# Kernel optimization log

Measured on AMD Instinct MI355X. Metric: run time of the kernel, lower is better.

The kernel has to match this reference:

```python
import jax, jax.numpy as jnp
import numpy as np

N = 320
C_Z = 128
H = 4
C_H = 32


def setup_inputs() -> dict:
    key = jax.random.key(0)
    ks = jax.random.split(key, 9)
    s = 0.02
    return {
        "x_normed": jax.random.normal(ks[0], (1, N, N, C_Z), dtype=jnp.float32),
        "triangle_bias": jax.random.normal(ks[1], (1, 1, H, N, N), dtype=jnp.float32),
        "wq": jax.random.normal(ks[2], (C_Z, H * C_H), dtype=jnp.float32) * s,
        "wk": jax.random.normal(ks[3], (C_Z, H * C_H), dtype=jnp.float32) * s,
        "wv": jax.random.normal(ks[4], (C_Z, H * C_H), dtype=jnp.float32) * s,
        "wg": jax.random.normal(ks[5], (C_Z, H * C_H), dtype=jnp.float32) * s,
        "bg": jnp.ones((H * C_H,), dtype=jnp.float32),  # OpenFold gating bias init = 1
        "wo": jax.random.normal(ks[6], (H * C_H, C_Z), dtype=jnp.float32) * s,
        "bo": jnp.zeros((C_Z,), dtype=jnp.float32),
    }


def reference(x_normed, triangle_bias, wq, wk, wv, wg, bg, wo, bo):
    b, n, m, cz = x_normed.shape  # [1, N, N, C_Z]
    # q/k/v projections (no bias, per OpenFold Attention)
    q = (x_normed @ wq).reshape(b, n, m, H, C_H) / np.sqrt(C_H)
    k = (x_normed @ wk).reshape(b, n, m, H, C_H)
    v = (x_normed @ wv).reshape(b, n, m, H, C_H)
    # attention over the last row dim; first N is a batch dim.
    # scores: [b, n, H, q, k]; triangle_bias [1, 1, H, N, N] broadcasts over n.
    scores = jnp.einsum("bnqhc,bnkhc->bnhqk", q, k) + triangle_bias
    a = jax.nn.softmax(scores, axis=-1)
    o = jnp.einsum("bnhqk,bnkhc->bnqhc", a, v)
    # sigmoid output gating
    g = jax.nn.sigmoid((x_normed @ wg + bg).reshape(b, n, m, H, C_H))
    o = o * g
    out = o.reshape(b, n, m, H * C_H) @ wo + bo
    return out
```

## Files before the change

kernel.cpp:

```cpp
#include <hip/hip_runtime.h>

typedef __bf16 bf16;
typedef __bf16 bf16x8 __attribute__((ext_vector_type(8)));
typedef __bf16 bf16x4 __attribute__((ext_vector_type(4)));
typedef __bf16 bf16x2 __attribute__((ext_vector_type(2)));
typedef float  f32x4  __attribute__((ext_vector_type(4)));
typedef unsigned int u32;
typedef u32 u32x4 __attribute__((ext_vector_type(4)));

#define NN_  320
#define CZ_  128
#define H_   4
#define CH_  32
#define LOG2E_ 1.4426950408889634f

__device__ __forceinline__ u32 pack_bf16(float a, float b) {
    bf16x2 t; t[0] = (bf16)a; t[1] = (bf16)b;
    return __builtin_bit_cast(u32, t);
}

__global__ __launch_bounds__(512) void qkvg_kernel(
    const float* __restrict__ x,
    const float* __restrict__ wq, const float* __restrict__ wk,
    const float* __restrict__ wv, const float* __restrict__ wg,
    const float* __restrict__ bg,
    bf16* __restrict__ Qp, bf16* __restrict__ Kp,
    bf16* __restrict__ Vp, bf16* __restrict__ Gp)
{
    __shared__ bf16 wl[128][136];
    const int tid  = threadIdx.x;
    const int lane = tid & 63, wid = tid >> 6;
    const int l15  = lane & 15, l4 = lane >> 4;
    const int m0   = blockIdx.x << 7;

    const int arow = m0 + wid * 16 + l15;
    bf16x8 xf[4];
    #pragma unroll
    for (int ks = 0; ks < 4; ++ks) {
        float4 f0 = *reinterpret_cast<const float4*>(x + (size_t)arow * CZ_ + ks * 32 + l4 * 8);
        float4 f1 = *reinterpret_cast<const float4*>(x + (size_t)arow * CZ_ + ks * 32 + l4 * 8 + 4);
        bf16x8 t;
        t[0]=(bf16)f0.x; t[1]=(bf16)f0.y; t[2]=(bf16)f0.z; t[3]=(bf16)f0.w;
        t[4]=(bf16)f1.x; t[5]=(bf16)f1.y; t[6]=(bf16)f1.z; t[7]=(bf16)f1.w;
        xf[ks] = t;
    }

    int nQ[4], qQ[4];
    #pragma unroll
    for (int r = 0; r < 4; ++r) {
        int m = m0 + wid * 16 + l4 * 4 + r;
        nQ[r] = m / NN_; qQ[r] = m - nQ[r] * NN_;
    }
    const int nV = arow / NN_, qV = arow - nV * NN_;

    const float* Ws[4] = {wq, wk, wv, wg};
    #pragma unroll
    for (int mat = 0; mat < 4; ++mat) {
        __syncthreads();
        const float* w = Ws[mat];
        #pragma unroll
        for (int it = 0; it < 8; ++it) {
            int u  = tid + (it << 9);
            int j  = u & 127, k4 = u >> 7;
            bf16x4 t;
            t[0] = (bf16)w[(k4 * 4 + 0) * CZ_ + j];
            t[1] = (bf16)w[(k4 * 4 + 1) * CZ_ + j];
            t[2] = (bf16)w[(k4 * 4 + 2) * CZ_ + j];
            t[3] = (bf16)w[(k4 * 4 + 3) * CZ_ + j];
            *reinterpret_cast<bf16x4*>(&wl[j][k4 * 4]) = t;
        }
        __syncthreads();

        f32x4 zero = {0.f, 0.f, 0.f, 0.f};
        f32x4 acc[8];
        #pragma unroll
        for (int ct = 0; ct < 8; ++ct) acc[ct] = zero;

        #pragma unroll
        for (int ks = 0; ks < 4; ++ks) {
            #pragma unroll
            for (int ct = 0; ct < 8; ++ct) {
                bf16x8 wf = *reinterpret_cast<const bf16x8*>(&wl[ct * 16 + l15][ks * 32 + l4 * 8]);
                if (mat == 2)
                    acc[ct] = __builtin_amdgcn_mfma_f32_16x16x32_bf16(wf, xf[ks], acc[ct], 0, 0, 0);
                else
                    acc[ct] = __builtin_amdgcn_mfma_f32_16x16x32_bf16(xf[ks], wf, acc[ct], 0, 0, 0);
            }
        }

        if (mat == 0) {
            #pragma unroll
            for (int ct = 0; ct < 8; ++ct) {
                const int cout = ct * 16 + l15, hh = cout >> 5, cc = cout & 31;
                #pragma unroll
                for (int r = 0; r < 4; ++r)
                    Qp[(size_t)((nQ[r] * H_ + hh) * NN_ + qQ[r]) * CH_ + cc] =
                        (bf16)(acc[ct][r] * 0.25500003540695464f);
            }
        } else if (mat == 1) {
            #pragma unroll
            for (int ct = 0; ct < 8; ++ct) {
                const int cout = ct * 16 + l15, hh = cout >> 5, cc = cout & 31;
                #pragma unroll
                for (int r = 0; r < 4; ++r)
                    Kp[(size_t)((nQ[r] * H_ + hh) * NN_ + qQ[r]) * CH_ + cc] = (bf16)acc[ct][r];
            }
        } else if (mat == 2) {
            #pragma unroll
            for (int ct = 0; ct < 8; ++ct) {
                #pragma unroll
                for (int r = 0; r < 4; ++r) {
                    const int cout = ct * 16 + l4 * 4 + r, hh = cout >> 5, cc = cout & 31;
                    Vp[(size_t)((nV * H_ + hh) * CH_ + cc) * NN_ + qV] = (bf16)acc[ct][r];
                }
            }
        } else {
            #pragma unroll
            for (int ct = 0; ct < 8; ++ct) {
                const int cout = ct * 16 + l15;
                const float bgj = bg[cout];
                #pragma unroll
                for (int r = 0; r < 4; ++r) {
                    float t = acc[ct][r] + bgj;
                    Gp[(size_t)(m0 + wid * 16 + l4 * 4 + r) * CZ_ + cout] =
                        (bf16)(1.0f / (1.0f + __expf(-t)));
                }
            }
        }
    }
}

__global__ __launch_bounds__(640, 2) void attn_kernel(
    const bf16* __restrict__ Qp, const bf16* __restrict__ Kp,
    const bf16* __restrict__ Vp, bf16* __restrict__ Gp,
    const float* __restrict__ bias)
{
    __shared__ bf16 Kl[320][40];
    __shared__ bf16 Vl[32][344];
    const int tid  = threadIdx.x;
    const int lane = tid & 63;
    const int wid  = tid >> 6;
    const int l15  = lane & 15, l4 = lane >> 4;
    const int gid = blockIdx.x;
    const int lin = (gid & 7) * 160 + (gid >> 3);
    const int h   = lin / NN_;
    const int n   = lin - h * NN_;

    const size_t nh = (size_t)(n * H_ + h);
    const bf16* Kh = Kp + nh * NN_ * CH_;
    const bf16* Vh = Vp + nh * CH_ * NN_;
    const bf16* Qh = Qp + nh * NN_ * CH_;

    #pragma unroll
    for (int i = 0; i < 2; ++i) {
        int c  = tid + i * 640;
        int kr = c >> 2, kc = (c & 3) * 8;
        *reinterpret_cast<bf16x8*>(&Kl[kr][kc]) =
            *reinterpret_cast<const bf16x8*>(Kh + kr * CH_ + kc);
        int vr = c / 40, vc = (c % 40) * 8;
        *reinterpret_cast<bf16x8*>(&Vl[vr][vc]) =
            *reinterpret_cast<const bf16x8*>(Vh + vr * NN_ + vc);
    }
    __syncthreads();

    const f32x4 zero = {0.f, 0.f, 0.f, 0.f};
    bf16x8 onesf;
    #pragma unroll
    for (int i = 0; i < 8; ++i) onesf[i] = (bf16)1.0f;

    #pragma unroll 1
    for (int qg = 0; qg < 2; ++qg) {
        const int qb = wid * 32 + qg * 16;
        const bf16x8 qf = *reinterpret_cast<const bf16x8*>(&Qh[(qb + l15) * CH_ + l4 * 8]);
        const float* bq = bias + ((size_t)h * NN_ + qb + l15) * NN_ + l4 * 4;
        const size_t gbase = ((size_t)n * NN_ + qb + l15) * CZ_ + h * CH_;
        const bf16x4 g0 = *reinterpret_cast<const bf16x4*>(&Gp[gbase + l4 * 4]);
        const bf16x4 g1 = *reinterpret_cast<const bf16x4*>(&Gp[gbase + 16 + l4 * 4]);

        f32x4 o0 = zero, o1 = zero, ol = zero;

        float4 bA0 = *reinterpret_cast<const float4*>(bq);
        float4 bA1 = *reinterpret_cast<const float4*>(bq + 16);
        float4 bB0 = *reinterpret_cast<const float4*>(bq + 32);
        float4 bB1 = *reinterpret_cast<const float4*>(bq + 48);

#define ATTN_TP(TP, B0, B1, PRE)                                                   \
    {                                                                              \
        const int kvm = (TP) * 32;                                                 \
        bf16x8 kf0 = *reinterpret_cast<const bf16x8*>(&Kl[kvm + l15][l4 * 8]);     \
        bf16x8 kf1 = *reinterpret_cast<const bf16x8*>(&Kl[kvm + 16 + l15][l4 * 8]);\
        __builtin_amdgcn_s_setprio(1);                                             \
        f32x4 s0 = __builtin_amdgcn_mfma_f32_16x16x32_bf16(kf0, qf, zero, 0, 0, 0);\
        f32x4 s1 = __builtin_amdgcn_mfma_f32_16x16x32_bf16(kf1, qf, zero, 0, 0, 0);\
        __builtin_amdgcn_s_setprio(0);                                             \
        float p0 = __builtin_amdgcn_exp2f(__builtin_fmaf(B0.x, LOG2E_, s0[0]));    \
        float p1 = __builtin_amdgcn_exp2f(__builtin_fmaf(B0.y, LOG2E_, s0[1]));    \
        float p2 = __builtin_amdgcn_exp2f(__builtin_fmaf(B0.z, LOG2E_, s0[2]));    \
        float p3 = __builtin_amdgcn_exp2f(__builtin_fmaf(B0.w, LOG2E_, s0[3]));    \
        float p4 = __builtin_amdgcn_exp2f(__builtin_fmaf(B1.x, LOG2E_, s1[0]));    \
        float p5 = __builtin_amdgcn_exp2f(__builtin_fmaf(B1.y, LOG2E_, s1[1]));    \
        float p6 = __builtin_amdgcn_exp2f(__builtin_fmaf(B1.z, LOG2E_, s1[2]));    \
        float p7 = __builtin_amdgcn_exp2f(__builtin_fmaf(B1.w, LOG2E_, s1[3]));    \
        u32x4 ww;                                                                  \
        ww[0] = pack_bf16(p0, p1); ww[1] = pack_bf16(p2, p3);                      \
        ww[2] = pack_bf16(p4, p5); ww[3] = pack_bf16(p6, p7);                      \
        bf16x8 pf = __builtin_bit_cast(bf16x8, ww);                                \
        if (PRE) {                                            \
            B0 = *reinterpret_cast<const float4*>(bq + ((TP) + 2) * 32);           \
            B1 = *reinterpret_cast<const float4*>(bq + ((TP) + 2) * 32 + 16);      \
        }                                                                          \
        bf16x4 va0 = *reinterpret_cast<const bf16x4*>(&Vl[l15][kvm + l4 * 4]);     \
        bf16x4 va1 = *reinterpret_cast<const bf16x4*>(&Vl[l15][kvm + 16 + l4 * 4]);\
        bf16x4 vb0 = *reinterpret_cast<const bf16x4*>(&Vl[16 + l15][kvm + l4 * 4]);\
        bf16x4 vb1 = *reinterpret_cast<const bf16x4*>(&Vl[16 + l15][kvm + 16 + l4 * 4]); \
        bf16x8 vf0 = __builtin_shufflevector(va0, va1, 0, 1, 2, 3, 4, 5, 6, 7);    \
        bf16x8 vf1 = __builtin_shufflevector(vb0, vb1, 0, 1, 2, 3, 4, 5, 6, 7);    \
        __builtin_amdgcn_s_setprio(1);                                             \
        ol = __builtin_amdgcn_mfma_f32_16x16x32_bf16(onesf, pf, ol, 0, 0, 0);      \
        o0 = __builtin_amdgcn_mfma_f32_16x16x32_bf16(vf0, pf, o0, 0, 0, 0);        \
        o1 = __builtin_amdgcn_mfma_f32_16x16x32_bf16(vf1, pf, o1, 0, 0, 0);        \
        __builtin_amdgcn_s_setprio(0);                                             \
    }

        #pragma unroll 1
        for (int t2 = 0; t2 < 4; ++t2) {
            ATTN_TP(2 * t2,     bA0, bA1, true);
            ATTN_TP(2 * t2 + 1, bB0, bB1, true);
        }
        ATTN_TP(8, bA0, bA1, false);
        ATTN_TP(9, bB0, bB1, false);
#undef ATTN_TP

        const float linv = 1.0f / ol[0];

        bf16x4 h0, h1;
        #pragma unroll
        for (int r = 0; r < 4; ++r) {
            h0[r] = (bf16)(o0[r] * linv * (float)g0[r]);
            h1[r] = (bf16)(o1[r] * linv * (float)g1[r]);
        }
        *reinterpret_cast<bf16x4*>(&Gp[gbase + l4 * 4]) = h0;
        *reinterpret_cast<bf16x4*>(&Gp[gbase + 16 + l4 * 4]) = h1;
    }
}

__global__ __launch_bounds__(512) void oproj_kernel(
    const bf16* __restrict__ og, const float* __restrict__ wo,
    const float* __restrict__ bo, float* __restrict__ out)
{
    __shared__ bf16 wl[128][136];
    const int tid  = threadIdx.x;
    const int lane = tid & 63, wid = tid >> 6;
    const int l15  = lane & 15, l4 = lane >> 4;
    const int m0   = blockIdx.x << 7;

    #pragma unroll
    for (int it = 0; it < 8; ++it) {
        int u  = tid + (it << 9);
        int j  = u & 127, k4 = u >> 7;
        bf16x4 t;
        t[0] = (bf16)wo[(k4 * 4 + 0) * CZ_ + j];
        t[1] = (bf16)wo[(k4 * 4 + 1) * CZ_ + j];
        t[2] = (bf16)wo[(k4 * 4 + 2) * CZ_ + j];
        t[3] = (bf16)wo[(k4 * 4 + 3) * CZ_ + j];
        *reinterpret_cast<bf16x4*>(&wl[j][k4 * 4]) = t;
    }
    __syncthreads();

    const int arow = m0 + wid * 16 + l15;
    bf16x8 af[4];
    #pragma unroll
    for (int ks = 0; ks < 4; ++ks)
        af[ks] = *reinterpret_cast<const bf16x8*>(&og[(size_t)arow * CZ_ + ks * 32 + l4 * 8]);

    f32x4 zero = {0.f, 0.f, 0.f, 0.f};
    f32x4 acc[8];
    #pragma unroll
    for (int ct = 0; ct < 8; ++ct) acc[ct] = zero;
    #pragma unroll
    for (int ks = 0; ks < 4; ++ks)
        #pragma unroll
        for (int ct = 0; ct < 8; ++ct) {
            bf16x8 wf = *reinterpret_cast<const bf16x8*>(&wl[ct * 16 + l15][ks * 32 + l4 * 8]);
            acc[ct] = __builtin_amdgcn_mfma_f32_16x16x32_bf16(af[ks], wf, acc[ct], 0, 0, 0);
        }

    #pragma unroll
    for (int ct = 0; ct < 8; ++ct) {
        const int cout = ct * 16 + l15;
        const float bov = bo[cout];
        #pragma unroll
        for (int r = 0; r < 4; ++r)
            out[(size_t)(m0 + wid * 16 + l4 * 4 + r) * CZ_ + cout] = acc[ct][r] + bov;
    }
}

extern "C" void kernel_launch(void* const* d_in, const int* in_sizes, int n_in,
                              void* d_out, int out_size, void* d_ws, size_t ws_size,
                              hipStream_t stream) {
    (void)in_sizes; (void)n_in; (void)out_size; (void)ws_size;
    const float* x    = (const float*)d_in[0];
    const float* bias = (const float*)d_in[1];
    const float* wq   = (const float*)d_in[2];
    const float* wk   = (const float*)d_in[3];
    const float* wv   = (const float*)d_in[4];
    const float* wg   = (const float*)d_in[5];
    const float* bg   = (const float*)d_in[6];
    const float* wo   = (const float*)d_in[7];
    const float* bo   = (const float*)d_in[8];
    float* out = (float*)d_out;

    const size_t ELEMS = (size_t)NN_ * NN_ * CZ_;
    bf16* Qp = (bf16*)d_ws;
    bf16* Gp = Qp + ELEMS;
    bf16* Kp = (bf16*)d_out;
    bf16* Vp = Kp + ELEMS;

    qkvg_kernel<<<dim3(800), 512, 0, stream>>>(x, wq, wk, wv, wg, bg, Qp, Kp, Vp, Gp);
    attn_kernel<<<dim3(1280), 640, 0, stream>>>(Qp, Kp, Vp, Gp, bias);
    oproj_kernel<<<dim3(800), 512, 0, stream>>>(Gp, wo, bo, out);
}
```

Measured before the change: 143.0 us.

## Split attention blocks by query half, prefetch weights, permute V smem layout

Software-prefetches the next projection weight matrix into registers while the current one is used in the QKVG kernel. The attention kernel is split so each block handles half the queries (2560 blocks, one 16-row group per wave). It raises the occupancy hint to 4 and stores V in LDS in a permuted layout so each fragment is one 8-wide load instead of two 4-wide loads plus a shuffle. The output projection now processes two 128-row tiles per block to amortize the weight staging. The trade-off is that K/V staging into LDS is duplicated across twice as many attention blocks, and the extra prefetch registers raise register pressure in the QKVG kernel.

```diff
diff --git a/kernel.cpp b/kernel.cpp
--- a/kernel.cpp
+++ b/kernel.cpp
@@ -54,22 +54,37 @@
     const int nV = arow / NN_, qV = arow - nV * NN_;
 
     const float* Ws[4] = {wq, wk, wv, wg};
+
+    float pw[8][4];
+    #pragma unroll
+    for (int it = 0; it < 8; ++it) {
+        const int u = tid + (it << 9), j = u & 127, k4 = u >> 7;
+        #pragma unroll
+        for (int r = 0; r < 4; ++r) pw[it][r] = wq[(k4 * 4 + r) * CZ_ + j];
+    }
+
     #pragma unroll
     for (int mat = 0; mat < 4; ++mat) {
         __syncthreads();
-        const float* w = Ws[mat];
         #pragma unroll
         for (int it = 0; it < 8; ++it) {
-            int u  = tid + (it << 9);
-            int j  = u & 127, k4 = u >> 7;
+            const int u = tid + (it << 9), j = u & 127, k4 = u >> 7;
             bf16x4 t;
-            t[0] = (bf16)w[(k4 * 4 + 0) * CZ_ + j];
-            t[1] = (bf16)w[(k4 * 4 + 1) * CZ_ + j];
-            t[2] = (bf16)w[(k4 * 4 + 2) * CZ_ + j];
-            t[3] = (bf16)w[(k4 * 4 + 3) * CZ_ + j];
+            t[0] = (bf16)pw[it][0]; t[1] = (bf16)pw[it][1];
+            t[2] = (bf16)pw[it][2]; t[3] = (bf16)pw[it][3];
             *reinterpret_cast<bf16x4*>(&wl[j][k4 * 4]) = t;
         }
         __syncthreads();
+
+        if (mat < 3) {
+            const float* wnext = Ws[mat + 1];
+            #pragma unroll
+            for (int it = 0; it < 8; ++it) {
+                const int u = tid + (it << 9), j = u & 127, k4 = u >> 7;
+                #pragma unroll
+                for (int r = 0; r < 4; ++r) pw[it][r] = wnext[(k4 * 4 + r) * CZ_ + j];
+            }
+        }
 
         f32x4 zero = {0.f, 0.f, 0.f, 0.f};
         f32x4 acc[8];
@@ -130,21 +145,23 @@
     }
 }
 
-__global__ __launch_bounds__(640, 2) void attn_kernel(
+__global__ __launch_bounds__(640, 4) void attn_kernel(
     const bf16* __restrict__ Qp, const bf16* __restrict__ Kp,
     const bf16* __restrict__ Vp, bf16* __restrict__ Gp,
     const float* __restrict__ bias)
 {
     __shared__ bf16 Kl[320][40];
-    __shared__ bf16 Vl[32][344];
+    __shared__ bf16 Vl[32][328];
     const int tid  = threadIdx.x;
     const int lane = tid & 63;
     const int wid  = tid >> 6;
     const int l15  = lane & 15, l4 = lane >> 4;
-    const int gid = blockIdx.x;
-    const int lin = (gid & 7) * 160 + (gid >> 3);
-    const int h   = lin / NN_;
-    const int n   = lin - h * NN_;
+    const int gid  = blockIdx.x;
+    const int lin  = (gid & 7) * 320 + (gid >> 3);
+    const int h    = lin / 640;
+    const int rem  = lin - h * 640;
+    const int n    = rem >> 1;
+    const int half = rem & 1;
 
     const size_t nh = (size_t)(n * H_ + h);
     const bf16* Kh = Kp + nh * NN_ * CH_;
@@ -157,9 +174,14 @@
         int kr = c >> 2, kc = (c & 3) * 8;
         *reinterpret_cast<bf16x8*>(&Kl[kr][kc]) =
             *reinterpret_cast<const bf16x8*>(Kh + kr * CH_ + kc);
-        int vr = c / 40, vc = (c % 40) * 8;
-        *reinterpret_cast<bf16x8*>(&Vl[vr][vc]) =
-            *reinterpret_cast<const bf16x8*>(Vh + vr * NN_ + vc);
+        int vr = c / 40, vc = c - vr * 40;
+        int m = vc & 3, b32 = vc >> 2;
+        bf16x8 g = *reinterpret_cast<const bf16x8*>(Vh + vr * NN_ + vc * 8);
+        int base = b32 * 32 + (m & 1) * 16 + (m >> 1) * 4;
+        bf16x4 lo; lo[0] = g[0]; lo[1] = g[1]; lo[2] = g[2]; lo[3] = g[3];
+        bf16x4 hi; hi[0] = g[4]; hi[1] = g[5]; hi[2] = g[6]; hi[3] = g[7];
+        *reinterpret_cast<bf16x4*>(&Vl[vr][base]) = lo;
+        *reinterpret_cast<bf16x4*>(&Vl[vr][base + 8]) = hi;
     }
     __syncthreads();
 
@@ -168,27 +190,27 @@
     #pragma unroll
     for (int i = 0; i < 8; ++i) onesf[i] = (bf16)1.0f;
 
-    #pragma unroll 1
-    for (int qg = 0; qg < 2; ++qg) {
-        const int qb = wid * 32 + qg * 16;
-        const bf16x8 qf = *reinterpret_cast<const bf16x8*>(&Qh[(qb + l15) * CH_ + l4 * 8]);
-        const float* bq = bias + ((size_t)h * NN_ + qb + l15) * NN_ + l4 * 4;
-        const size_t gbase = ((size_t)n * NN_ + qb + l15) * CZ_ + h * CH_;
-        const bf16x4 g0 = *reinterpret_cast<const bf16x4*>(&Gp[gbase + l4 * 4]);
-        const bf16x4 g1 = *reinterpret_cast<const bf16x4*>(&Gp[gbase + 16 + l4 * 4]);
-
-        f32x4 o0 = zero, o1 = zero, ol = zero;
-
-        float4 bA0 = *reinterpret_cast<const float4*>(bq);
-        float4 bA1 = *reinterpret_cast<const float4*>(bq + 16);
-        float4 bB0 = *reinterpret_cast<const float4*>(bq + 32);
-        float4 bB1 = *reinterpret_cast<const float4*>(bq + 48);
+    const int qb = half * 160 + wid * 16;
+    const bf16x8 qf = *reinterpret_cast<const bf16x8*>(&Qh[(qb + l15) * CH_ + l4 * 8]);
+    const float* bq = bias + ((size_t)h * NN_ + qb + l15) * NN_ + l4 * 4;
+    const size_t gbase = ((size_t)n * NN_ + qb + l15) * CZ_ + h * CH_;
+    const bf16x4 g0 = *reinterpret_cast<const bf16x4*>(&Gp[gbase + l4 * 4]);
+    const bf16x4 g1 = *reinterpret_cast<const bf16x4*>(&Gp[gbase + 16 + l4 * 4]);
+
+    f32x4 o0 = zero, o1 = zero, ol = zero;
+
+    float4 bA0 = *reinterpret_cast<const float4*>(bq);
+    float4 bA1 = *reinterpret_cast<const float4*>(bq + 16);
+    float4 bB0 = *reinterpret_cast<const float4*>(bq + 32);
+    float4 bB1 = *reinterpret_cast<const float4*>(bq + 48);
 
 #define ATTN_TP(TP, B0, B1, PRE)                                                   \
     {                                                                              \
         const int kvm = (TP) * 32;                                                 \
         bf16x8 kf0 = *reinterpret_cast<const bf16x8*>(&Kl[kvm + l15][l4 * 8]);     \
         bf16x8 kf1 = *reinterpret_cast<const bf16x8*>(&Kl[kvm + 16 + l15][l4 * 8]);\
+        bf16x8 vf0 = *reinterpret_cast<const bf16x8*>(&Vl[l15][kvm + l4 * 8]);     \
+        bf16x8 vf1 = *reinterpret_cast<const bf16x8*>(&Vl[16 + l15][kvm + l4 * 8]);\
         __builtin_amdgcn_s_setprio(1);                                             \
         f32x4 s0 = __builtin_amdgcn_mfma_f32_16x16x32_bf16(kf0, qf, zero, 0, 0, 0);\
         f32x4 s1 = __builtin_amdgcn_mfma_f32_16x16x32_bf16(kf1, qf, zero, 0, 0, 0);\
@@ -209,12 +231,6 @@
             B0 = *reinterpret_cast<const float4*>(bq + ((TP) + 2) * 32);           \
             B1 = *reinterpret_cast<const float4*>(bq + ((TP) + 2) * 32 + 16);      \
         }                                                                          \
-        bf16x4 va0 = *reinterpret_cast<const bf16x4*>(&Vl[l15][kvm + l4 * 4]);     \
-        bf16x4 va1 = *reinterpret_cast<const bf16x4*>(&Vl[l15][kvm + 16 + l4 * 4]);\
-        bf16x4 vb0 = *reinterpret_cast<const bf16x4*>(&Vl[16 + l15][kvm + l4 * 4]);\
-        bf16x4 vb1 = *reinterpret_cast<const bf16x4*>(&Vl[16 + l15][kvm + 16 + l4 * 4]); \
-        bf16x8 vf0 = __builtin_shufflevector(va0, va1, 0, 1, 2, 3, 4, 5, 6, 7);    \
-        bf16x8 vf1 = __builtin_shufflevector(vb0, vb1, 0, 1, 2, 3, 4, 5, 6, 7);    \
         __builtin_amdgcn_s_setprio(1);                                             \
         ol = __builtin_amdgcn_mfma_f32_16x16x32_bf16(onesf, pf, ol, 0, 0, 0);      \
         o0 = __builtin_amdgcn_mfma_f32_16x16x32_bf16(vf0, pf, o0, 0, 0, 0);        \
@@ -222,26 +238,24 @@
         __builtin_amdgcn_s_setprio(0);                                             \
     }
 
-        #pragma unroll 1
-        for (int t2 = 0; t2 < 4; ++t2) {
-            ATTN_TP(2 * t2,     bA0, bA1, true);
-            ATTN_TP(2 * t2 + 1, bB0, bB1, true);
-        }
-        ATTN_TP(8, bA0, bA1, false);
-        ATTN_TP(9, bB0, bB1, false);
+    #pragma unroll 1
+    for (int t2 = 0; t2 < 4; ++t2) {
+        ATTN_TP(2 * t2,     bA0, bA1, true);
+        ATTN_TP(2 * t2 + 1, bB0, bB1, true);
+    }
+    ATTN_TP(8, bA0, bA1, false);
+    ATTN_TP(9, bB0, bB1, false);
 #undef ATTN_TP
 
-        const float linv = 1.0f / ol[0];
-
-        bf16x4 h0, h1;
-        #pragma unroll
-        for (int r = 0; r < 4; ++r) {
-            h0[r] = (bf16)(o0[r] * linv * (float)g0[r]);
-            h1[r] = (bf16)(o1[r] * linv * (float)g1[r]);
-        }
-        *reinterpret_cast<bf16x4*>(&Gp[gbase + l4 * 4]) = h0;
-        *reinterpret_cast<bf16x4*>(&Gp[gbase + 16 + l4 * 4]) = h1;
-    }
+    const float linv = 1.0f / ol[0];
+    bf16x4 h0, h1;
+    #pragma unroll
+    for (int r = 0; r < 4; ++r) {
+        h0[r] = (bf16)(o0[r] * linv * (float)g0[r]);
+        h1[r] = (bf16)(o1[r] * linv * (float)g1[r]);
+    }
+    *reinterpret_cast<bf16x4*>(&Gp[gbase + l4 * 4]) = h0;
+    *reinterpret_cast<bf16x4*>(&Gp[gbase + 16 + l4 * 4]) = h1;
 }
 
 __global__ __launch_bounds__(512) void oproj_kernel(
@@ -252,7 +266,6 @@
     const int tid  = threadIdx.x;
     const int lane = tid & 63, wid = tid >> 6;
     const int l15  = lane & 15, l4 = lane >> 4;
-    const int m0   = blockIdx.x << 7;
 
     #pragma unroll
     for (int it = 0; it < 8; ++it) {
@@ -267,31 +280,35 @@
     }
     __syncthreads();
 
-    const int arow = m0 + wid * 16 + l15;
-    bf16x8 af[4];
-    #pragma unroll
-    for (int ks = 0; ks < 4; ++ks)
-        af[ks] = *reinterpret_cast<const bf16x8*>(&og[(size_t)arow * CZ_ + ks * 32 + l4 * 8]);
-
-    f32x4 zero = {0.f, 0.f, 0.f, 0.f};
-    f32x4 acc[8];
-    #pragma unroll
-    for (int ct = 0; ct < 8; ++ct) acc[ct] = zero;
-    #pragma unroll
-    for (int ks = 0; ks < 4; ++ks)
+    #pragma unroll 1
+    for (int rt = 0; rt < 2; ++rt) {
+        const int m0 = (blockIdx.x << 8) + rt * 128;
+        const int arow = m0 + wid * 16 + l15;
+        bf16x8 af[4];
+        #pragma unroll
+        for (int ks = 0; ks < 4; ++ks)
+            af[ks] = *reinterpret_cast<const bf16x8*>(&og[(size_t)arow * CZ_ + ks * 32 + l4 * 8]);
+
+        f32x4 zero = {0.f, 0.f, 0.f, 0.f};
+        f32x4 acc[8];
+        #pragma unroll
+        for (int ct = 0; ct < 8; ++ct) acc[ct] = zero;
+        #pragma unroll
+        for (int ks = 0; ks < 4; ++ks)
+            #pragma unroll
+            for (int ct = 0; ct < 8; ++ct) {
+                bf16x8 wf = *reinterpret_cast<const bf16x8*>(&wl[ct * 16 + l15][ks * 32 + l4 * 8]);
+                acc[ct] = __builtin_amdgcn_mfma_f32_16x16x32_bf16(af[ks], wf, acc[ct], 0, 0, 0);
+            }
+
         #pragma unroll
         for (int ct = 0; ct < 8; ++ct) {
-            bf16x8 wf = *reinterpret_cast<const bf16x8*>(&wl[ct * 16 + l15][ks * 32 + l4 * 8]);
-            acc[ct] = __builtin_amdgcn_mfma_f32_16x16x32_bf16(af[ks], wf, acc[ct], 0, 0, 0);
-        }
-
-    #pragma unroll
-    for (int ct = 0; ct < 8; ++ct) {
-        const int cout = ct * 16 + l15;
-        const float bov = bo[cout];
-        #pragma unroll
-        for (int r = 0; r < 4; ++r)
-            out[(size_t)(m0 + wid * 16 + l4 * 4 + r) * CZ_ + cout] = acc[ct][r] + bov;
+            const int cout = ct * 16 + l15;
+            const float bov = bo[cout];
+            #pragma unroll
+            for (int r = 0; r < 4; ++r)
+                out[(size_t)(m0 + wid * 16 + l4 * 4 + r) * CZ_ + cout] = acc[ct][r] + bov;
+        }
     }
 }
 
@@ -317,6 +334,6 @@
     bf16* Vp = Kp + ELEMS;
 
     qkvg_kernel<<<dim3(800), 512, 0, stream>>>(x, wq, wk, wv, wg, bg, Qp, Kp, Vp, Gp);
-    attn_kernel<<<dim3(1280), 640, 0, stream>>>(Qp, Kp, Vp, Gp, bias);
-    oproj_kernel<<<dim3(800), 512, 0, stream>>>(Gp, wo, bo, out);
-}
+    attn_kernel<<<dim3(2560), 640, 0, stream>>>(Qp, Kp, Vp, Gp, bias);
+    oproj_kernel<<<dim3(400), 512, 0, stream>>>(Gp, wo, bo, out);
+}
```

Measured after the change: 142.1 us. About the same (-0.6%).
